# Performance work log

Hardware: AMD Instinct MI355X
Metric: run time of the kernel (lower is better)

## Reference

```python
import jax, jax.numpy as jnp
import numpy as np
from jax import lax

B, IMG, P, D, DEPTH = 32, 512, 16, 256, 8
G = IMG // P            # 32 grid side
N = G * G               # 1024 tokens
DQ = D // 8             # 32 (CCNet-style reduced q/k dim)
DF = 4 * D

# fixed Laplacian kernel for EdgeTokenExtractor (depthwise, HWIO with I=1)
_LAP = np.array([[0., -1., 0.], [-1., 4., -1.], [0., -1., 0.]], np.float32)


def setup_inputs() -> dict:
    key = jax.random.key(0)
    ks = jax.random.split(key, 16)
    s = 0.02
    return {
        'x': jax.random.normal(ks[0], (B, 1, IMG, IMG), jnp.float32),
        'w_patch': jax.random.normal(ks[1], (D, 1, P, P), jnp.float32) * s,
        'b_patch': jnp.zeros((D,), jnp.float32),
        'pos': jax.random.normal(ks[2], (1, N, D), jnp.float32) * s,
        'w_edge': jax.random.normal(ks[3], (D, D), jnp.float32) * s,
        'b_edge': jnp.zeros((D,), jnp.float32),
        'ln_g': jnp.ones((DEPTH, D), jnp.float32),
        'ln_b': jnp.zeros((DEPTH, D), jnp.float32),
        'wq': jax.random.normal(ks[4], (DEPTH, D, DQ), jnp.float32) * s,
        'bq': jnp.zeros((DEPTH, DQ), jnp.float32),
        'wk': jax.random.normal(ks[5], (DEPTH, D, DQ), jnp.float32) * s,
        'bk': jnp.zeros((DEPTH, DQ), jnp.float32),
        'wv': jax.random.normal(ks[6], (DEPTH, D, D), jnp.float32) * s,
        'bv': jnp.zeros((DEPTH, D), jnp.float32),
        'gamma': jnp.full((DEPTH,), 0.1, jnp.float32),
        'w1': jax.random.normal(ks[7], (DEPTH, D, DF), jnp.float32) * s,
        'b1': jnp.zeros((DEPTH, DF), jnp.float32),
        'w2': jax.random.normal(ks[8], (DEPTH, DF, D), jnp.float32) * s,
        'b2': jnp.zeros((DEPTH, D), jnp.float32),
        'w_head': jax.random.normal(ks[9], (D, 1), jnp.float32) * s,
        'b_head': jnp.zeros((1,), jnp.float32),
    }


def _ln(x, g, b):
    m = x.mean(-1, keepdims=True)
    v = ((x - m) ** 2).mean(-1, keepdims=True)
    return (x - m) * lax.rsqrt(v + 1e-5) * g + b


def _criss_cross(xn, wq, bq, wk, bk, wv, bv, gamma):
    # xn: [B,N,D] -> grid [B,G,G,D]; each token attends to its row + column.
    b_ = xn.shape[0]
    grid = xn.reshape(b_, G, G, D)
    q = grid @ wq + bq            # [B,G,G,DQ]
    k = grid @ wk + bk
    v = grid @ wv + bv            # [B,G,G,D]
    scale = 1.0 / np.sqrt(DQ).astype(np.float32)
    row = jnp.einsum('bhwc,bhvc->bhwv', q, k) * scale   # attend along width
    col = jnp.einsum('bhwc,buwc->bhwu', q, k) * scale   # attend along height
    # mask the duplicated self position in the column branch (CCNet trick)
    col = col - 1e9 * jnp.eye(G, dtype=col.dtype)[:, None, :]
    a = jax.nn.softmax(jnp.concatenate([row, col], axis=-1), axis=-1)  # [B,G,G,2G]
    out = (jnp.einsum('bhwv,bhvc->bhwc', a[..., :G], v)
           + jnp.einsum('bhwu,buwc->bhwc', a[..., G:], v))
    return (gamma * out + grid).reshape(b_, N, D)


def _edge_tokens(t, w_edge, b_edge):
    # depthwise Laplacian over the token grid, then linear + tanh
    b_ = t.shape[0]
    grid = t.reshape(b_, G, G, D)
    kern = jnp.tile(jnp.asarray(_LAP).reshape(3, 3, 1, 1), (1, 1, 1, D))  # [3,3,1,D]
    e = lax.conv_general_dilated(grid, kern, (1, 1), 'SAME',
                                 dimension_numbers=('NHWC', 'HWIO', 'NHWC'),
                                 feature_group_count=D)
    return jnp.tanh(e.reshape(b_, N, D) @ w_edge + b_edge)


def reference(x, w_patch, b_patch, pos, w_edge, b_edge, ln_g, ln_b,
              wq, bq, wk, bk, wv, bv, gamma, w1, b1, w2, b2, w_head, b_head):
    b_ = x.shape[0]
    # patch embed: conv stride=patch -> [B,D,G,G] -> [B,N,D]
    t = lax.conv_general_dilated(x, w_patch, (P, P), 'VALID',
                                 dimension_numbers=('NCHW', 'OIHW', 'NCHW'))
    t = t + b_patch[None, :, None, None]
    t = t.reshape(b_, D, N).transpose(0, 2, 1)
    t = t + pos
    t = t + _edge_tokens(t, w_edge, b_edge)

    def block(h, p):
        lg, lb, wq_, bq_, wk_, bk_, wv_, bv_, gm, w1_, b1_, w2_, b2_ = p
        # NOTE: original block reuses the SAME LayerNorm params for both sublayers
        h = h + _criss_cross(_ln(h, lg, lb), wq_, bq_, wk_, bk_, wv_, bv_, gm)
        hn = _ln(h, lg, lb)
        h = h + jax.nn.gelu(hn @ w1_ + b1_, approximate=False) @ w2_ + b2_
        return h, None

    t, _ = lax.scan(block, t, (ln_g, ln_b, wq, bq, wk, bk, wv, bv, gamma, w1, b1, w2, b2))
    out = t @ w_head + b_head                      # [B,N,1]
    return out.transpose(0, 2, 1).reshape(b_, 1, G, G)
```

## Files before the change

### kernel.cpp

```cpp
#include <hip/hip_runtime.h>
#include <hip/hip_bf16.h>

#define BB   32
#define IMG  512
#define PP   16
#define DD   256
#define GG   32
#define NN   1024
#define DQ_  32
#define DF_  1024
#define DEPTH_ 8

using short8  = __attribute__((ext_vector_type(8))) short;
using floatx4 = __attribute__((ext_vector_type(4))) float;

__device__ __forceinline__ float bu2f(unsigned short u) {
    return __uint_as_float(((unsigned int)u) << 16);
}
__device__ __forceinline__ unsigned short f2b(float f) {
    unsigned int u = __float_as_uint(f);
    u += 0x7fffu + ((u >> 16) & 1u);
    return (unsigned short)(u >> 16);
}
__device__ __forceinline__ unsigned int pack2(float a, float b) {
    return (unsigned int)f2b(a) | ((unsigned int)f2b(b) << 16);
}
__device__ __forceinline__ float gelu_fast(float x) {
    float u = 0.7978845608028654f * (x + 0.044715f * x * x * x);
    float t = 1.f - 2.f / (1.f + __expf(2.f * u));
    return 0.5f * x * (1.0f + t);
}
__device__ __forceinline__ float lo16(unsigned int u) {
    return __uint_as_float(u << 16);
}
__device__ __forceinline__ float hi16(unsigned int u) {
    return __uint_as_float(u & 0xffff0000u);
}
__device__ __forceinline__ float dot8(uint4 a, uint4 b) {
    const unsigned int* pa = (const unsigned int*)&a;
    const unsigned int* pb = (const unsigned int*)&b;
    float s = 0.f;
    #pragma unroll
    for (int i = 0; i < 4; ++i)
        s += lo16(pa[i]) * lo16(pb[i]) + hi16(pa[i]) * hi16(pb[i]);
    return s;
}

__global__ __launch_bounds__(256) void k_wtrans(const float* __restrict__ in,
                                                unsigned short* __restrict__ out,
                                                int R, int C) {
    __shared__ float tile[32][33];
    const int l = blockIdx.z;
    const int r0 = blockIdx.x * 32, c0 = blockIdx.y * 32;
    const int tx = threadIdx.x & 31, ty = threadIdx.x >> 5;
    const float* src = in + (size_t)l * R * C;
    unsigned short* dst = out + (size_t)l * R * C;
    #pragma unroll
    for (int i = 0; i < 4; ++i)
        tile[ty + i * 8][tx] = src[(size_t)(r0 + ty + i * 8) * C + c0 + tx];
    __syncthreads();
    #pragma unroll
    for (int i = 0; i < 4; ++i)
        dst[(size_t)(c0 + ty + i * 8) * R + r0 + tx] = f2b(tile[tx][ty + i * 8]);
}

__global__ __launch_bounds__(256) void k_qktrans(const float* __restrict__ wq,
                                                 const float* __restrict__ wk,
                                                 unsigned short* __restrict__ o) {
    const int l = blockIdx.z, j = blockIdx.x, k = threadIdx.x;
    float v = (j < 32) ? wq[(size_t)l * 8192 + k * 32 + j]
                       : wk[(size_t)l * 8192 + k * 32 + (j - 32)];
    o[((size_t)l * 64 + j) * 256 + k] = f2b(v);
}

__global__ void k_bqk(const float* __restrict__ bq, const float* __restrict__ bk,
                      float* __restrict__ o) {
    const int l = blockIdx.x, j = threadIdx.x;
    o[l * 64 + j] = (j < 32) ? bq[l * 32 + j] : bk[l * 32 + (j - 32)];
}

__global__ __launch_bounds__(256) void k_cvt(const float* __restrict__ in,
                                             unsigned short* __restrict__ out) {
    int i = blockIdx.x * 256 + threadIdx.x;
    out[i] = f2b(in[i]);
}

__global__ __launch_bounds__(256) void k_im2col(const float* __restrict__ x,
                                                unsigned short* __restrict__ xp) {
    const int tok = blockIdx.x;
    const int b  = tok >> 10;
    const int n  = tok & (NN - 1);
    const int gi = n >> 5, gj = n & 31;
    const int pi = threadIdx.x >> 4, pj = threadIdx.x & 15;
    xp[(size_t)tok * 256 + threadIdx.x] =
        f2b(x[(size_t)(b * IMG + gi * PP + pi) * IMG + gj * PP + pj]);
}

template <int K, int N, int MODE>
__global__ __launch_bounds__(256) void k_gemm(
    const unsigned short* __restrict__ A, const unsigned short* __restrict__ Bt,
    const float* __restrict__ bias, unsigned short* __restrict__ Cb,
    float* __restrict__ Cf, const float* __restrict__ pos) {
    __shared__ alignas(16) unsigned short As[64 * 32];
    __shared__ alignas(16) unsigned short Bs[64 * 32];
    const int t  = threadIdx.x;
    const int m0 = blockIdx.x * 64, n0 = blockIdx.y * 64;
    const int row = t >> 2, ch = t & 3;
    const unsigned short* ga = A  + (size_t)(m0 + row) * K + ch * 8;
    const unsigned short* gb = Bt + (size_t)(n0 + row) * K + ch * 8;

    const int lane = t & 63, wid = t >> 6;
    const int quad = lane >> 4, r = lane & 15;
    const int wm = (wid >> 1) * 32, wn = (wid & 1) * 32;

    floatx4 acc00 = {0.f, 0.f, 0.f, 0.f}, acc01 = {0.f, 0.f, 0.f, 0.f};
    floatx4 acc10 = {0.f, 0.f, 0.f, 0.f}, acc11 = {0.f, 0.f, 0.f, 0.f};

    uint4 ra = *(const uint4*)ga;
    uint4 rb = *(const uint4*)gb;
    const int KS = K / 32;
    for (int ks = 0; ks < KS; ++ks) {
        __syncthreads();
        *(uint4*)&As[t * 8] = ra;
        *(uint4*)&Bs[t * 8] = rb;
        __syncthreads();
        if (ks + 1 < KS) {
            ra = *(const uint4*)(ga + (ks + 1) * 32);
            rb = *(const uint4*)(gb + (ks + 1) * 32);
        }
        short8 a0 = *(const short8*)&As[(wm + r) * 32 + quad * 8];
        short8 a1 = *(const short8*)&As[(wm + 16 + r) * 32 + quad * 8];
        short8 b0 = *(const short8*)&Bs[(wn + r) * 32 + quad * 8];
        short8 b1 = *(const short8*)&Bs[(wn + 16 + r) * 32 + quad * 8];
        acc00 = __builtin_amdgcn_mfma_f32_16x16x32_bf16(a0, b0, acc00, 0, 0, 0);
        acc01 = __builtin_amdgcn_mfma_f32_16x16x32_bf16(a0, b1, acc01, 0, 0, 0);
        acc10 = __builtin_amdgcn_mfma_f32_16x16x32_bf16(a1, b0, acc10, 0, 0, 0);
        acc11 = __builtin_amdgcn_mfma_f32_16x16x32_bf16(a1, b1, acc11, 0, 0, 0);
    }
    const int nA = n0 + wn + r;
    const int nB = nA + 16;
    const float bias0 = bias[nA], bias1 = bias[nB];
    #pragma unroll
    for (int i = 0; i < 2; ++i) {
        floatx4 aj0 = i ? acc10 : acc00;
        floatx4 aj1 = i ? acc11 : acc01;
        const int mb = m0 + wm + i * 16 + quad * 4;
        #pragma unroll
        for (int g = 0; g < 4; ++g) {
            const int m = mb + g;
            float v0 = aj0[g] + bias0, v1 = aj1[g] + bias1;
            if (MODE == 0) {
                Cb[(size_t)m * N + nA] = f2b(gelu_fast(v0));
                Cb[(size_t)m * N + nB] = f2b(gelu_fast(v1));
            } else if (MODE == 1) {
                Cf[(size_t)m * N + nA] += v0;
                Cf[(size_t)m * N + nB] += v1;
            } else if (MODE == 2) {
                Cb[(size_t)m * N + nA] = f2b(v0);
                Cb[(size_t)m * N + nB] = f2b(v1);
            } else if (MODE == 3) {
                Cf[(size_t)m * N + nA] += tanhf(v0);
                Cf[(size_t)m * N + nB] += tanhf(v1);
            } else {
                Cf[(size_t)m * N + nA] = v0 + pos[(size_t)(m & (NN - 1)) * N + nA];
                Cf[(size_t)m * N + nB] = v1 + pos[(size_t)(m & (NN - 1)) * N + nB];
            }
        }
    }
}

__global__ __launch_bounds__(256) void k_lap(const float* __restrict__ h,
                                             unsigned short* __restrict__ e) {
    int idx = blockIdx.x * 256 + threadIdx.x;
    int n  = (idx >> 8) & (NN - 1);
    int gi = n >> 5, gj = n & 31;
    float c  = h[idx];
    float up = (gi > 0)  ? h[idx - GG * DD] : 0.f;
    float dn = (gi < 31) ? h[idx + GG * DD] : 0.f;
    float lf = (gj > 0)  ? h[idx - DD] : 0.f;
    float rt = (gj < 31) ? h[idx + DD] : 0.f;
    e[idx] = f2b(4.f * c - up - dn - lf - rt);
}

__global__ __launch_bounds__(256) void k_ln(
    const float* __restrict__ h, const float* __restrict__ g,
    const float* __restrict__ b, unsigned short* __restrict__ xnb, int layer) {
    const int wid = threadIdx.x >> 6, lane = threadIdx.x & 63;
    const int row = blockIdx.x * 4 + wid;
    const float4 xv = *(const float4*)(h + (size_t)row * DD + lane * 4);
    float s = xv.x + xv.y + xv.z + xv.w;
    #pragma unroll
    for (int o = 32; o; o >>= 1) s += __shfl_xor(s, o, 64);
    const float m = s * (1.f / 256.f);
    float t0 = xv.x - m, t1 = xv.y - m, t2 = xv.z - m, t3 = xv.w - m;
    float s2 = t0 * t0 + t1 * t1 + t2 * t2 + t3 * t3;
    #pragma unroll
    for (int o = 32; o; o >>= 1) s2 += __shfl_xor(s2, o, 64);
    const float r = rsqrtf(s2 * (1.f / 256.f) + 1e-5f);
    const int d0 = lane * 4;
    const float4 gv = *(const float4*)(g + layer * DD + d0);
    const float4 bv = *(const float4*)(b + layer * DD + d0);
    uint2 outp;
    outp.x = pack2(t0 * r * gv.x + bv.x, t1 * r * gv.y + bv.y);
    outp.y = pack2(t2 * r * gv.z + bv.z, t3 * r * gv.w + bv.w);
    *(uint2*)(xnb + (size_t)row * DD + d0) = outp;
}

__global__ __launch_bounds__(256) void k_score(
    const unsigned short* __restrict__ qkb, unsigned short* __restrict__ P) {
    const int wid = threadIdx.x >> 6, lane = threadIdx.x & 63;
    const int tok = blockIdx.x * 4 + wid;
    const int b = tok >> 10, n = tok & (NN - 1);
    const int gi = n >> 5, gj = n & 31;
    const uint4* qp = (const uint4*)(qkb + (size_t)tok * 64);
    uint4 q0 = qp[0], q1 = qp[1], q2 = qp[2], q3 = qp[3];
    const int key = (lane < 32) ? (b * NN + gi * 32 + lane)
                                : (b * NN + (lane - 32) * 32 + gj);
    const uint4* kp = (const uint4*)(qkb + (size_t)key * 64 + 32);
    uint4 k0 = kp[0], k1 = kp[1], k2 = kp[2], k3 = kp[3];
    float s = dot8(q0, k0) + dot8(q1, k1) + dot8(q2, k2) + dot8(q3, k3);
    s *= 0.17677669529663687f;
    if (lane >= 32 && (lane - 32) == gi) s -= 1e9f;
    float m = s;
    #pragma unroll
    for (int o = 32; o; o >>= 1) m = fmaxf(m, __shfl_xor(m, o, 64));
    float e = expf(s - m);
    float sum = e;
    #pragma unroll
    for (int o = 32; o; o >>= 1) sum += __shfl_xor(sum, o, 64);
    P[(size_t)tok * 64 + lane] = f2b(e / sum);
}

__global__ __launch_bounds__(256) void k_avcol(
    const unsigned short* __restrict__ P, const unsigned short* __restrict__ v,
    float* __restrict__ h, const float* __restrict__ gamma, int layer) {
    const int idx = blockIdx.x;
    const int b = idx >> 7, gj = (idx >> 2) & 31, oct = idx & 3;
    const int wid = threadIdx.x >> 6, lane = threadIdx.x & 63;
    const int d0 = lane * 4;
    uint2 vr[32];
    const unsigned short* vbase = v + ((size_t)(b * NN + gj)) * 256 + d0;
    #pragma unroll
    for (int u = 0; u < 32; ++u)
        vr[u] = *(const uint2*)(vbase + (size_t)u * 32 * 256);
    const float g = gamma[layer];
    size_t hidx[2];
    float4 hv[2];
    unsigned int pa[2][16];
    #pragma unroll
    for (int jj = 0; jj < 2; ++jj) {
        const int gi = oct * 8 + wid * 2 + jj;
        const int tok = b * NN + gi * 32 + gj;
        hidx[jj] = (size_t)tok * 256 + d0;
        const uint4* pp = (const uint4*)(P + (size_t)tok * 64 + 32);
        *(uint4*)(pa[jj])      = pp[0];
        *(uint4*)(pa[jj] + 4)  = pp[1];
        *(uint4*)(pa[jj] + 8)  = pp[2];
        *(uint4*)(pa[jj] + 12) = pp[3];
        hv[jj] = *(const float4*)(h + hidx[jj]);
    }
    #pragma unroll
    for (int jj = 0; jj < 2; ++jj) {
        float o0 = 0.f, o1 = 0.f, o2 = 0.f, o3 = 0.f;
        #pragma unroll
        for (int u = 0; u < 32; ++u) {
            float p = (u & 1) ? hi16(pa[jj][u >> 1]) : lo16(pa[jj][u >> 1]);
            o0 += p * lo16(vr[u].x); o1 += p * hi16(vr[u].x);
            o2 += p * lo16(vr[u].y); o3 += p * hi16(vr[u].y);
        }
        float4 r = hv[jj];
        r.x += g * o0; r.y += g * o1; r.z += g * o2; r.w += g * o3;
        *(float4*)(h + hidx[jj]) = r;
    }
}

__global__ __launch_bounds__(256) void k_avrow_ln(
    const unsigned short* __restrict__ P, const unsigned short* __restrict__ v,
    float* __restrict__ h, unsigned short* __restrict__ xnb,
    const float* __restrict__ gamma, const float* __restrict__ lg,
    const float* __restrict__ lb, int layer) {
    const int idx = blockIdx.x;
    const int b = idx >> 7, gi = (idx >> 2) & 31, oct = idx & 3;
    const int wid = threadIdx.x >> 6, lane = threadIdx.x & 63;
    const int d0 = lane * 4;
    uint2 vr[32];
    const unsigned short* vbase = v + ((size_t)(b * NN + gi * 32)) * 256 + d0;
    #pragma unroll
    for (int w = 0; w < 32; ++w)
        vr[w] = *(const uint2*)(vbase + (size_t)w * 256);
    const float g = gamma[layer];
    const float4 gv = *(const float4*)(lg + layer * DD + d0);
    const float4 bv = *(const float4*)(lb + layer * DD + d0);
    size_t hidx[2];
    float4 hv[2];
    uint2 xu[2];
    unsigned int pa[2][16];
    #pragma unroll
    for (int jj = 0; jj < 2; ++jj) {
        const int gj = oct * 8 + wid * 2 + jj;
        const int tok = b * NN + gi * 32 + gj;
        hidx[jj] = (size_t)tok * 256 + d0;
        const uint4* pp = (const uint4*)(P + (size_t)tok * 64);
        *(uint4*)(pa[jj])      = pp[0];
        *(uint4*)(pa[jj] + 4)  = pp[1];
        *(uint4*)(pa[jj] + 8)  = pp[2];
        *(uint4*)(pa[jj] + 12) = pp[3];
        hv[jj] = *(const float4*)(h + hidx[jj]);
        xu[jj] = *(const uint2*)(xnb + hidx[jj]);
    }
    #pragma unroll
    for (int jj = 0; jj < 2; ++jj) {
        float o0 = 0.f, o1 = 0.f, o2 = 0.f, o3 = 0.f;
        #pragma unroll
        for (int w = 0; w < 32; ++w) {
            float p = (w & 1) ? hi16(pa[jj][w >> 1]) : lo16(pa[jj][w >> 1]);
            o0 += p * lo16(vr[w].x); o1 += p * hi16(vr[w].x);
            o2 += p * lo16(vr[w].y); o3 += p * hi16(vr[w].y);
        }
        float f0 = hv[jj].x + lo16(xu[jj].x) + g * o0;
        float f1 = hv[jj].y + hi16(xu[jj].x) + g * o1;
        float f2 = hv[jj].z + lo16(xu[jj].y) + g * o2;
        float f3 = hv[jj].w + hi16(xu[jj].y) + g * o3;
        float s = f0 + f1 + f2 + f3;
        #pragma unroll
        for (int o = 32; o; o >>= 1) s += __shfl_xor(s, o, 64);
        const float m = s * (1.f / 256.f);
        float t0 = f0 - m, t1 = f1 - m, t2 = f2 - m, t3 = f3 - m;
        float s2 = t0 * t0 + t1 * t1 + t2 * t2 + t3 * t3;
        #pragma unroll
        for (int o = 32; o; o >>= 1) s2 += __shfl_xor(s2, o, 64);
        const float r = rsqrtf(s2 * (1.f / 256.f) + 1e-5f);
        float4 hvout = {f0, f1, f2, f3};
        *(float4*)(h + hidx[jj]) = hvout;
        uint2 outp;
        outp.x = pack2(t0 * r * gv.x + bv.x, t1 * r * gv.y + bv.y);
        outp.y = pack2(t2 * r * gv.z + bv.z, t3 * r * gv.w + bv.w);
        *(uint2*)(xnb + hidx[jj]) = outp;
    }
}

__global__ __launch_bounds__(256) void k_head(
    const float* __restrict__ h, const float* __restrict__ wh,
    const float* __restrict__ bh, float* __restrict__ out) {
    const int tok  = blockIdx.x * 4 + (threadIdx.x >> 6);
    const int lane = threadIdx.x & 63;
    float acc = 0.f;
    #pragma unroll
    for (int i = 0; i < 4; ++i)
        acc += h[(size_t)tok * DD + lane + 64 * i] * wh[lane + 64 * i];
    #pragma unroll
    for (int o = 32; o; o >>= 1) acc += __shfl_down(acc, o, 64);
    if (lane == 0) out[tok] = acc + bh[0];
}

extern "C" void kernel_launch(void* const* d_in, const int* in_sizes, int n_in,
                              void* d_out, int out_size, void* d_ws, size_t ws_size,
                              hipStream_t stream) {
    const float* fx   = (const float*)d_in[0];
    const float* fwp  = (const float*)d_in[1];
    const float* fbp  = (const float*)d_in[2];
    const float* fpos = (const float*)d_in[3];
    const float* fwe  = (const float*)d_in[4];
    const float* fbe  = (const float*)d_in[5];
    const float* flg  = (const float*)d_in[6];
    const float* flb  = (const float*)d_in[7];
    const float* fwq  = (const float*)d_in[8];
    const float* fbq  = (const float*)d_in[9];
    const float* fwk  = (const float*)d_in[10];
    const float* fbk  = (const float*)d_in[11];
    const float* fwv  = (const float*)d_in[12];
    const float* fbv  = (const float*)d_in[13];
    const float* fgam = (const float*)d_in[14];
    const float* fw1  = (const float*)d_in[15];
    const float* fb1  = (const float*)d_in[16];
    const float* fw2  = (const float*)d_in[17];
    const float* fb2  = (const float*)d_in[18];
    const float* fwh  = (const float*)d_in[19];
    const float* fbh  = (const float*)d_in[20];
    float* out = (float*)d_out;

    float* ws = (float*)d_ws;
    float*          h    = ws;
    unsigned short* xnb  = (unsigned short*)(ws + 8388608);
    unsigned short* w1t  = (unsigned short*)(ws + 12582912);
    unsigned short* w2t  = (unsigned short*)(ws + 13631488);
    unsigned short* wvT  = (unsigned short*)(ws + 14680064);
    unsigned short* wqkT = (unsigned short*)(ws + 14942208);
    unsigned short* wpb  = (unsigned short*)(ws + 15007744);
    unsigned short* weT  = (unsigned short*)(ws + 15040512);
    float*          bqk  = ws + 15073280;
    float* S = ws + 15073792;
    unsigned short* qkb  = (unsigned short*)S;
    unsigned short* v    = (unsigned short*)(S + 1048576);
    unsigned short* P    = (unsigned short*)(S + 5242880);
    unsigned short* xp   = (unsigned short*)S;
    unsigned short* e    = (unsigned short*)S;
    unsigned short* Hc   = (unsigned short*)S;

    const int TOK = BB * NN;

    k_wtrans<<<dim3(8, 32, 8), 256, 0, stream>>>(fw1, w1t, 256, 1024);
    k_wtrans<<<dim3(32, 8, 8), 256, 0, stream>>>(fw2, w2t, 1024, 256);
    k_wtrans<<<dim3(8, 8, 8),  256, 0, stream>>>(fwv, wvT, 256, 256);
    k_wtrans<<<dim3(8, 8, 1),  256, 0, stream>>>(fwe, weT, 256, 256);
    k_qktrans<<<dim3(64, 1, 8), 256, 0, stream>>>(fwq, fwk, wqkT);
    k_bqk<<<8, 64, 0, stream>>>(fbq, fbk, bqk);
    k_cvt<<<256, 256, 0, stream>>>(fwp, wpb);

    k_im2col<<<TOK, 256, 0, stream>>>(fx, xp);
    k_gemm<256, 256, 4><<<dim3(512, 4), 256, 0, stream>>>(
        xp, wpb, fbp, nullptr, h, fpos);
    k_lap<<<TOK, 256, 0, stream>>>(h, e);
    k_gemm<256, 256, 3><<<dim3(512, 4), 256, 0, stream>>>(
        e, weT, fbe, nullptr, h, nullptr);

    for (int l = 0; l < DEPTH_; ++l) {
        k_ln<<<TOK / 4, 256, 0, stream>>>(h, flg, flb, xnb, l);
        k_gemm<256, 64, 2><<<dim3(512, 1), 256, 0, stream>>>(
            xnb, wqkT + (size_t)l * 16384, bqk + l * 64, qkb, nullptr, nullptr);
        k_gemm<256, 256, 2><<<dim3(512, 4), 256, 0, stream>>>(
            xnb, wvT + (size_t)l * 65536, fbv + l * 256, v, nullptr, nullptr);
        k_score<<<TOK / 4, 256, 0, stream>>>(qkb, P);
        k_avcol<<<4096, 256, 0, stream>>>(P, v, h, fgam, l);
        k_avrow_ln<<<4096, 256, 0, stream>>>(P, v, h, xnb, fgam, flg, flb, l);
        for (int c = 0; c < 2; ++c) {
            k_gemm<256, 1024, 0><<<dim3(256, 16), 256, 0, stream>>>(
                xnb + (size_t)c * 16384 * 256, w1t + (size_t)l * 262144,
                fb1 + (size_t)l * 1024, Hc, nullptr, nullptr);
            k_gemm<1024, 256, 1><<<dim3(256, 4), 256, 0, stream>>>(
                Hc, w2t + (size_t)l * 262144,
                fb2 + (size_t)l * 256, nullptr, h + (size_t)c * 16384 * 256, nullptr);
        }
    }

    k_head<<<TOK / 4, 256, 0, stream>>>(h, fwh, fbh, out);
}
```

Before: 1.793 ms.

## Fuse Q/K/V projections into one GEMM and widen FFN1 tile to 64x128

Concatenates the Q, K and V weights and biases into one transposed bf16 matrix so each layer runs a single QKV GEMM launch. A new epilogue mode splits its output into the qk buffer and the v buffer. Adds a k_gemm_w kernel with 64x128 tiles, where each wave computes 32x64 with eight MFMA accumulators, and uses it for the FFN up-projection to improve A-tile reuse and halve the block count. In exchange the wider tile needs more registers and LDS per block, which may lower occupancy.

```diff
diff --git a/kernel.cpp b/kernel.cpp
--- a/kernel.cpp
+++ b/kernel.cpp
@@ -64,19 +64,26 @@
         dst[(size_t)(c0 + ty + i * 8) * R + r0 + tx] = f2b(tile[tx][ty + i * 8]);
 }
 
-__global__ __launch_bounds__(256) void k_qktrans(const float* __restrict__ wq,
-                                                 const float* __restrict__ wk,
-                                                 unsigned short* __restrict__ o) {
+__global__ __launch_bounds__(256) void k_qkvtrans(const float* __restrict__ wq,
+                                                  const float* __restrict__ wk,
+                                                  const float* __restrict__ wv,
+                                                  unsigned short* __restrict__ o) {
     const int l = blockIdx.z, j = blockIdx.x, k = threadIdx.x;
-    float v = (j < 32) ? wq[(size_t)l * 8192 + k * 32 + j]
-                       : wk[(size_t)l * 8192 + k * 32 + (j - 32)];
-    o[((size_t)l * 64 + j) * 256 + k] = f2b(v);
-}
-
-__global__ void k_bqk(const float* __restrict__ bq, const float* __restrict__ bk,
-                      float* __restrict__ o) {
+    float v;
+    if (j < 32)       v = wq[(size_t)l * 8192 + k * 32 + j];
+    else if (j < 64)  v = wk[(size_t)l * 8192 + k * 32 + (j - 32)];
+    else              v = wv[(size_t)l * 65536 + k * 256 + (j - 64)];
+    o[((size_t)l * 320 + j) * 256 + k] = f2b(v);
+}
+
+__global__ void k_bqkv(const float* __restrict__ bq, const float* __restrict__ bk,
+                       const float* __restrict__ bv, float* __restrict__ o) {
     const int l = blockIdx.x, j = threadIdx.x;
-    o[l * 64 + j] = (j < 32) ? bq[l * 32 + j] : bk[l * 32 + (j - 32)];
+    float r;
+    if (j < 32)      r = bq[l * 32 + j];
+    else if (j < 64) r = bk[l * 32 + (j - 32)];
+    else             r = bv[l * 256 + (j - 64)];
+    o[l * 320 + j] = r;
 }
 
 __global__ __launch_bounds__(256) void k_cvt(const float* __restrict__ in,
@@ -100,7 +107,8 @@
 __global__ __launch_bounds__(256) void k_gemm(
     const unsigned short* __restrict__ A, const unsigned short* __restrict__ Bt,
     const float* __restrict__ bias, unsigned short* __restrict__ Cb,
-    float* __restrict__ Cf, const float* __restrict__ pos) {
+    float* __restrict__ Cf, const float* __restrict__ pos,
+    unsigned short* __restrict__ Cb2) {
     __shared__ alignas(16) unsigned short As[64 * 32];
     __shared__ alignas(16) unsigned short Bs[64 * 32];
     const int t  = threadIdx.x;
@@ -161,9 +169,87 @@
             } else if (MODE == 3) {
                 Cf[(size_t)m * N + nA] += tanhf(v0);
                 Cf[(size_t)m * N + nB] += tanhf(v1);
-            } else {
+            } else if (MODE == 4) {
                 Cf[(size_t)m * N + nA] = v0 + pos[(size_t)(m & (NN - 1)) * N + nA];
                 Cf[(size_t)m * N + nB] = v1 + pos[(size_t)(m & (NN - 1)) * N + nB];
+            } else {
+                if (n0 == 0) {
+                    Cb[(size_t)m * 64 + nA] = f2b(v0);
+                    Cb[(size_t)m * 64 + nB] = f2b(v1);
+                } else {
+                    Cb2[(size_t)m * 256 + (nA - 64)] = f2b(v0);
+                    Cb2[(size_t)m * 256 + (nB - 64)] = f2b(v1);
+                }
+            }
+        }
+    }
+}
+
+template <int K, int N, int MODE>
+__global__ __launch_bounds__(256) void k_gemm_w(
+    const unsigned short* __restrict__ A, const unsigned short* __restrict__ Bt,
+    const float* __restrict__ bias, unsigned short* __restrict__ Cb,
+    float* __restrict__ Cf) {
+    __shared__ alignas(16) unsigned short As[64 * 32];
+    __shared__ alignas(16) unsigned short Bs[128 * 32];
+    const int t  = threadIdx.x;
+    const int m0 = blockIdx.x * 64, n0 = blockIdx.y * 128;
+    const int row = t >> 2, ch = t & 3;
+    const unsigned short* ga  = A  + (size_t)(m0 + row) * K + ch * 8;
+    const unsigned short* gb0 = Bt + (size_t)(n0 + row) * K + ch * 8;
+    const unsigned short* gb1 = Bt + (size_t)(n0 + 64 + row) * K + ch * 8;
+
+    const int lane = t & 63, wid = t >> 6;
+    const int quad = lane >> 4, r = lane & 15;
+    const int wm = (wid >> 1) * 32, wn = (wid & 1) * 64;
+
+    floatx4 acc[2][4];
+    #pragma unroll
+    for (int i = 0; i < 2; ++i)
+        #pragma unroll
+        for (int n = 0; n < 4; ++n) acc[i][n] = floatx4{0.f, 0.f, 0.f, 0.f};
+
+    uint4 ra  = *(const uint4*)ga;
+    uint4 rb0 = *(const uint4*)gb0;
+    uint4 rb1 = *(const uint4*)gb1;
+    const int KS = K / 32;
+    for (int ks = 0; ks < KS; ++ks) {
+        __syncthreads();
+        *(uint4*)&As[t * 8] = ra;
+        *(uint4*)&Bs[t * 8] = rb0;
+        *(uint4*)&Bs[2048 + t * 8] = rb1;
+        __syncthreads();
+        if (ks + 1 < KS) {
+            ra  = *(const uint4*)(ga  + (ks + 1) * 32);
+            rb0 = *(const uint4*)(gb0 + (ks + 1) * 32);
+            rb1 = *(const uint4*)(gb1 + (ks + 1) * 32);
+        }
+        short8 a0 = *(const short8*)&As[(wm + r) * 32 + quad * 8];
+        short8 a1 = *(const short8*)&As[(wm + 16 + r) * 32 + quad * 8];
+        short8 b[4];
+        #pragma unroll
+        for (int n = 0; n < 4; ++n)
+            b[n] = *(const short8*)&Bs[(wn + n * 16 + r) * 32 + quad * 8];
+        #pragma unroll
+        for (int n = 0; n < 4; ++n) {
+            acc[0][n] = __builtin_amdgcn_mfma_f32_16x16x32_bf16(a0, b[n], acc[0][n], 0, 0, 0);
+            acc[1][n] = __builtin_amdgcn_mfma_f32_16x16x32_bf16(a1, b[n], acc[1][n], 0, 0, 0);
+        }
+    }
+    #pragma unroll
+    for (int n = 0; n < 4; ++n) {
+        const int col = n0 + wn + n * 16 + r;
+        const float bs = bias[col];
+        #pragma unroll
+        for (int i = 0; i < 2; ++i) {
+            const int mb = m0 + wm + i * 16 + quad * 4;
+            #pragma unroll
+            for (int g = 0; g < 4; ++g) {
+                const int m = mb + g;
+                float v0 = acc[i][n][g] + bs;
+                if (MODE == 0)      Cb[(size_t)m * N + col] = f2b(gelu_fast(v0));
+                else if (MODE == 1) Cf[(size_t)m * N + col] += v0;
+                else                Cb[(size_t)m * N + col] = f2b(v0);
             }
         }
     }
@@ -380,16 +466,15 @@
     float* out = (float*)d_out;
 
     float* ws = (float*)d_ws;
-    float*          h    = ws;
-    unsigned short* xnb  = (unsigned short*)(ws + 8388608);
-    unsigned short* w1t  = (unsigned short*)(ws + 12582912);
-    unsigned short* w2t  = (unsigned short*)(ws + 13631488);
-    unsigned short* wvT  = (unsigned short*)(ws + 14680064);
-    unsigned short* wqkT = (unsigned short*)(ws + 14942208);
-    unsigned short* wpb  = (unsigned short*)(ws + 15007744);
-    unsigned short* weT  = (unsigned short*)(ws + 15040512);
-    float*          bqk  = ws + 15073280;
-    float* S = ws + 15073792;
+    float*          h     = ws;
+    unsigned short* xnb   = (unsigned short*)(ws + 8388608);
+    unsigned short* w1t   = (unsigned short*)(ws + 12582912);
+    unsigned short* w2t   = (unsigned short*)(ws + 13631488);
+    unsigned short* wqkvT = (unsigned short*)(ws + 14680064);
+    unsigned short* wpb   = (unsigned short*)(ws + 15007744);
+    unsigned short* weT   = (unsigned short*)(ws + 15040512);
+    float*          bqkv  = ws + 15073280;
+    float* S = ws + 15075840;
     unsigned short* qkb  = (unsigned short*)S;
     unsigned short* v    = (unsigned short*)(S + 1048576);
     unsigned short* P    = (unsigned short*)(S + 5242880);
@@ -401,35 +486,34 @@
 
     k_wtrans<<<dim3(8, 32, 8), 256, 0, stream>>>(fw1, w1t, 256, 1024);
     k_wtrans<<<dim3(32, 8, 8), 256, 0, stream>>>(fw2, w2t, 1024, 256);
-    k_wtrans<<<dim3(8, 8, 8),  256, 0, stream>>>(fwv, wvT, 256, 256);
     k_wtrans<<<dim3(8, 8, 1),  256, 0, stream>>>(fwe, weT, 256, 256);
-    k_qktrans<<<dim3(64, 1, 8), 256, 0, stream>>>(fwq, fwk, wqkT);
-    k_bqk<<<8, 64, 0, stream>>>(fbq, fbk, bqk);
+    k_qkvtrans<<<dim3(320, 1, 8), 256, 0, stream>>>(fwq, fwk, fwv, wqkvT);
+    k_bqkv<<<8, 320, 0, stream>>>(fbq, fbk, fbv, bqkv);
     k_cvt<<<256, 256, 0, stream>>>(fwp, wpb);
 
     k_im2col<<<TOK, 256, 0, stream>>>(fx, xp);
     k_gemm<256, 256, 4><<<dim3(512, 4), 256, 0, stream>>>(
-        xp, wpb, fbp, nullptr, h, fpos);
+        xp, wpb, fbp, nullptr, h, fpos, nullptr);
     k_lap<<<TOK, 256, 0, stream>>>(h, e);
     k_gemm<256, 256, 3><<<dim3(512, 4), 256, 0, stream>>>(
-        e, weT, fbe, nullptr, h, nullptr);
+        e, weT, fbe, nullptr, h, nullptr, nullptr);
 
     for (int l = 0; l < DEPTH_; ++l) {
         k_ln<<<TOK / 4, 256, 0, stream>>>(h, flg, flb, xnb, l);
-        k_gemm<256, 64, 2><<<dim3(512, 1), 256, 0, stream>>>(
-            xnb, wqkT + (size_t)l * 16384, bqk + l * 64, qkb, nullptr, nullptr);
-        k_gemm<256, 256, 2><<<dim3(512, 4), 256, 0, stream>>>(
-            xnb, wvT + (size_t)l * 65536, fbv + l * 256, v, nullptr, nullptr);
+        k_gemm<256, 320, 5><<<dim3(512, 5), 256, 0, stream>>>(
+            xnb, wqkvT + (size_t)l * 81920, bqkv + l * 320, qkb, nullptr,
+            nullptr, v);
         k_score<<<TOK / 4, 256, 0, stream>>>(qkb, P);
         k_avcol<<<4096, 256, 0, stream>>>(P, v, h, fgam, l);
         k_avrow_ln<<<4096, 256, 0, stream>>>(P, v, h, xnb, fgam, flg, flb, l);
         for (int c = 0; c < 2; ++c) {
-            k_gemm<256, 1024, 0><<<dim3(256, 16), 256, 0, stream>>>(
+            k_gemm_w<256, 1024, 0><<<dim3(256, 8), 256, 0, stream>>>(
                 xnb + (size_t)c * 16384 * 256, w1t + (size_t)l * 262144,
-                fb1 + (size_t)l * 1024, Hc, nullptr, nullptr);
+                fb1 + (size_t)l * 1024, Hc, nullptr);
             k_gemm<1024, 256, 1><<<dim3(256, 4), 256, 0, stream>>>(
                 Hc, w2t + (size_t)l * 262144,
-                fb2 + (size_t)l * 256, nullptr, h + (size_t)c * 16384 * 256, nullptr);
+                fb2 + (size_t)l * 256, nullptr, h + (size_t)c * 16384 * 256,
+                nullptr, nullptr);
         }
     }
 
```

After: 1.796 ms. About the same (+0.2%).
